# Kernel tuning notes

Measured on AMD Instinct MI355X. Metric: run time of the kernel, lower is better.

## Reference

```python
import jax, jax.numpy as jnp
import numpy as np

# ---- fixed architecture constants (from init_kwargs) ----
N_WALL, N_ROOF, N_WINDOW = 4, 1, 2
N_RC = N_WALL + N_ROOF
HID = 32
ENC_LEN = 48
DT = 900.0
R_OPAQUE, C_OPAQUE = 10.0, 1.0e5
R_TRANS = 2.0
DIRECT_COEF, ABS_WALL_COEF, ABS_ROOF_COEF = 0.5, 0.5, 0.5
C_ZONE = 1.0e5
B, T = 2048, 1440


def setup_inputs() -> dict:
    key = jax.random.key(0)
    k0, k1, k2 = jax.random.split(key, 3)
    input_X = jax.random.normal(k0, (B, T, 7), dtype=jnp.float32)
    # EnvelopeRC deterministic inits
    rc_R_inv = jnp.concatenate([
        1.0 / (10.0 + 1.0 * jnp.arange(N_WALL, dtype=jnp.float32)),
        1.0 / (20.0 + 2.0 * jnp.arange(N_ROOF, dtype=jnp.float32))])
    rc_C_inv = jnp.concatenate([
        1.0 / (80.0 + 10.0 * jnp.arange(N_WALL, dtype=jnp.float32)),
        1.0 / (60.0 + 10.0 * jnp.arange(N_ROOF, dtype=jnp.float32))])
    window_R_inv = 1.0 / (1.0 + 0.1 * jnp.arange(N_WINDOW, dtype=jnp.float32))
    # Internal MLP: xavier_uniform with gain 0.1, zero bias
    lim1 = 0.1 * np.sqrt(6.0 / (2 + HID))
    int_W1 = jax.random.uniform(k1, (HID, 2), jnp.float32, -lim1, lim1)
    int_b1 = jnp.zeros((HID,), jnp.float32)
    lim2 = 0.1 * np.sqrt(6.0 / (HID + 1))
    int_W2 = jax.random.uniform(k2, (1, HID), jnp.float32, -lim2, lim2)
    int_b2 = jnp.zeros((1,), jnp.float32)
    return {
        'input_X': input_X,
        'rc_R_inv': rc_R_inv, 'rc_C_inv': rc_C_inv, 'window_R_inv': window_R_inv,
        'hvac_gain': jnp.float32(0.1),
        'int_W1': int_W1, 'int_b1': int_b1, 'int_W2': int_W2, 'int_b2': int_b2,
        'int_gain': jnp.float32(0.1),
        'direct_gain': jnp.float32(0.1), 'abs_wall': jnp.float32(0.1), 'abs_roof': jnp.float32(0.1),
        'zone_C_inv': jnp.float32(1.0 / 10000.0),
    }


def _forward(input_X, rc_R_inv, rc_C_inv, window_R_inv, hvac_gain,
             int_W1, int_b1, int_W2, int_b2, int_gain,
             direct_gain, abs_wall, abs_roof, zone_C_inv):
    sp = jax.nn.softplus
    Bn, Tn = input_X.shape[0], input_X.shape[1]
    tz_gt  = input_X[:, :, 0]   # [B,T]
    t_amb  = input_X[:, :, 1]
    sol    = input_X[:, :, 2]
    int_x  = input_X[:, :, 3:6]
    hvac_x = input_X[:, :, 6]

    # Internal MLP (state-free -> vectorized over time)
    h1  = jax.nn.relu(jnp.einsum('bti,hi->bth', int_x[:, :, :2], int_W1) + int_b1)
    sch = jax.nn.sigmoid(jnp.einsum('bth,oh->bto', h1, int_W2) + int_b2)[:, :, 0] + int_x[:, :, 2]
    q_int  = sp(int_gain) * 0.1 * sch          # [B,T]
    q_hvac = sp(hvac_gain) * 0.1 * hvac_x      # [B,T]

    # Bounded RC parameters
    r_inv   = sp(rc_R_inv) * (1.0 / R_OPAQUE)  # [n_rc]
    c_inv   = sp(rc_C_inv) * (1.0 / C_OPAQUE)  # [n_rc]
    win_rsum = jnp.sum(sp(window_R_inv)) * (1.0 / R_TRANS)
    abs_rc  = jnp.where(jnp.arange(N_RC) < N_WALL,
                        sp(abs_wall) * ABS_WALL_COEF,
                        sp(abs_roof) * ABS_ROOF_COEF)   # [n_rc]
    q_dir   = sp(direct_gain) * DIRECT_COEF * sol       # [B,T]
    cz_inv  = sp(zone_C_inv) * (1.0 / C_ZONE)

    # Initial state: Tmid_i = 0.7*Tzone0 + 0.3*Tamb0
    Tz0   = tz_gt[:, 0]                                      # [B]
    Tmid0 = jnp.broadcast_to((0.7 * Tz0 + 0.3 * t_amb[:, 0])[:, None], (Bn, N_RC))

    # Teacher forcing during encoder window: carry GT zone temp while t+1 < enc_len
    tz_gt_next = jnp.concatenate([tz_gt[:, 1:], tz_gt[:, -1:]], axis=1)  # [B,T]
    use_gt = (jnp.arange(Tn) + 1) < ENC_LEN                              # [T]

    xs = (t_amb.T, sol.T, q_dir.T, q_int.T, q_hvac.T, tz_gt_next.T, use_gt)

    def step(carry, x):
        Tz, Tmid = carry                      # [B], [B,n_rc]
        ta, so, qd, qi, qh, gt_next, ug = x
        q_in  = (ta[:, None] - Tmid) * r_inv
        q_out = (Tmid - Tz[:, None]) * r_inv
        dTmid = (q_in - q_out + so[:, None] * abs_rc) * c_inv
        q_env = jnp.sum(q_out, axis=1) + (ta - Tz) * win_rsum
        dTz   = (q_env + qi + qh + qd) * cz_inv
        Tz_new   = Tz + dTz * DT
        Tmid_new = Tmid + dTmid * DT
        Tz_carry = jnp.where(ug, gt_next, Tz_new)
        return (Tz_carry, Tmid_new), Tz_new

    _, tz_seq = jax.lax.scan(step, (Tz0, Tmid0), xs)   # [T,B]
    return jnp.transpose(tz_seq)[:, :, None]           # [B,T,1]


def reference(input_X, rc_R_inv, rc_C_inv, window_R_inv, hvac_gain,
              int_W1, int_b1, int_W2, int_b2, int_gain,
              direct_gain, abs_wall, abs_roof, zone_C_inv):
    return _forward(input_X, rc_R_inv, rc_C_inv, window_R_inv, hvac_gain,
                    int_W1, int_b1, int_W2, int_b2, int_gain,
                    direct_gain, abs_wall, abs_roof, zone_C_inv)
```

## Files before the change

### kernel.cpp

```cpp
#include <hip/hip_runtime.h>
#include <math.h>

#define BATCH 2048
#define TLEN  1440
#define NC    30
#define CL    48

#define PACK_OFF 0
#define E_OFF    (BATCH*TLEN*4)
#define XC_OFF   (E_OFF + NC*6*BATCH)
#define A48_OFF  (XC_OFF + BATCH*NC*6)
#define VCOL_OFF (A48_OFF + 64)
#define PRM_OFF  (VCOL_OFF + 320)
#define WS_FLOATS (PRM_OFF + 32)

__device__ __forceinline__ float sp_precise(float x) { return log1pf(expf(x)); }

__global__ void k0_params(const float* __restrict__ rcR, const float* __restrict__ rcC,
                          const float* __restrict__ winR, const float* __restrict__ hvg,
                          const float* __restrict__ ing, const float* __restrict__ dg,
                          const float* __restrict__ aw, const float* __restrict__ ar,
                          const float* __restrict__ zc, float* __restrict__ ws) {
  __shared__ float A0s[36], Ma[36], Mb[36], M16[36], vbuf[2][8];
  int ln = threadIdx.x;
  float r[5], cc[5];
  #pragma unroll
  for (int j = 0; j < 5; ++j) { r[j] = sp_precise(rcR[j]) * 0.1f; cc[j] = sp_precise(rcC[j]) * 1e-5f; }
  float w    = (sp_precise(winR[0]) + sp_precise(winR[1])) * 0.5f;
  float cz   = sp_precise(zc[0]) * 1e-5f;
  float aW   = sp_precise(aw[0]) * 0.5f, aR = sp_precise(ar[0]) * 0.5f;
  float dtcz = 900.f * cz;
  if (ln == 0) {
    float* prm = ws + PRM_OFF;
    float rsum = 0.f;
    for (int j = 0; j < 5; ++j) {
      float P = 900.f * r[j] * cc[j];
      prm[j]      = P;
      prm[5 + j]  = 1.f - 2.f * P;
      prm[10 + j] = 900.f * cc[j] * ((j < 4) ? aW : aR);
      prm[15 + j] = dtcz * r[j];
      rsum += r[j];
    }
    prm[20] = 1.f - dtcz * (w + rsum);
    prm[21] = dtcz * w;
    prm[22] = dtcz;
    prm[23] = sp_precise(ing[0]) * 0.1f;
    prm[24] = sp_precise(hvg[0]) * 0.1f;
    prm[25] = sp_precise(dg[0])  * 0.5f;
    for (int i = 0; i < 36; ++i) A0s[i] = 0.f;
    A0s[0] = prm[20];
    for (int j = 0; j < 5; ++j) {
      A0s[0 * 6 + 1 + j]       = dtcz * r[j];
      A0s[(1 + j) * 6 + 0]     = prm[j];
      A0s[(1 + j) * 6 + 1 + j] = prm[5 + j];
    }
  }
  __syncthreads();
  int i6 = ln / 6, j6 = ln % 6;
  bool act = ln < 36;
#define MM(DST, L, R) { if (act) { float s = 0.f; \
  for (int m = 0; m < 6; ++m) s = fmaf((L)[i6 * 6 + m], (R)[m * 6 + j6], s); \
  (DST)[ln] = s; } __syncthreads(); }
  MM(Mb, A0s, A0s);
  MM(Ma, Mb, Mb);
  MM(Mb, Ma, Ma);
  MM(Ma, Mb, Mb);
  if (act) M16[ln] = Ma[ln];
  __syncthreads();
  MM(Mb, Ma, Ma);
  MM(Ma, Mb, M16);
  if (act) ws[A48_OFF + ln] = Ma[ln];
  if (ln < 6) vbuf[0][ln] = A0s[ln];
  __syncthreads();
  int cur = 0;
  for (int k = 0; k < CL; ++k) {
    if (ln < 6) {
      ws[VCOL_OFF + ln * CL + k] = vbuf[cur][ln];
      float s = 0.f;
      for (int m = 0; m < 6; ++m) s = fmaf(vbuf[cur][m], A0s[m * 6 + ln], s);
      vbuf[1 - cur][ln] = s;
    }
    __syncthreads();
    cur ^= 1;
  }
}

__global__ __launch_bounds__(256) void k1_pack(const float* __restrict__ X,
    const float* __restrict__ W1, const float* __restrict__ B1,
    const float* __restrict__ W2, const float* __restrict__ B2,
    float* __restrict__ ws) {
  int tid = blockIdx.x * 256 + threadIdx.x;
  const float* prm = ws + PRM_OFF;
  float dtczw = prm[21], dtcz = prm[22], cInt = prm[23], cHv = prm[24], cDir = prm[25];
  const float* x = X + (size_t)tid * 7;
  float ta = x[1], so = x[2], x3 = x[3], x4 = x[4], x5 = x[5], hv = x[6];
  float acc = B2[0];
  #pragma unroll
  for (int h = 0; h < 32; ++h) {
    float z = fmaf(W1[2 * h], x3, fmaf(W1[2 * h + 1], x4, B1[h]));
    acc = fmaf(W2[h], fmaxf(z, 0.f), acc);
  }
  float sch = __frcp_rn(1.f + __expf(-acc)) + x5;
  float q = fmaf(cInt, sch, fmaf(cHv, hv, cDir * so));
  float u = fmaf(dtczw, ta, dtcz * q);
  int b = tid / TLEN;
  int t = tid - b * TLEN;
  float gt = (t < 47) ? x[7] : 0.f;
  ((float4*)(ws + PACK_OFF))[tid] = make_float4(ta, so, u, gt);
}

__global__ __launch_bounds__(256) void k2a_scan(const float* __restrict__ X,
                                                float* __restrict__ out,
                                                float* __restrict__ ws) {
  int tid = blockIdx.x * 256 + threadIdx.x;
  int c = tid >> 11;
  int b = tid & (BATCH - 1);
  const float* prm = ws + PRM_OFF;
  float P0 = prm[0], P1 = prm[1], P2 = prm[2], P3 = prm[3], P4 = prm[4];
  float M0 = prm[5], M1 = prm[6], M2 = prm[7], M3 = prm[8], M4 = prm[9];
  float Q0 = prm[10], Q1 = prm[11], Q2 = prm[12], Q3 = prm[13], Q4 = prm[14];
  float K0 = prm[15], K1 = prm[16], K2 = prm[17], K3 = prm[18], K4 = prm[19];
  float AZ = prm[20];
  float Tz, T0, T1, T2, T3, T4;
  bool isc0 = (c == 0);
  if (isc0) {
    float tz0 = X[(size_t)b * (TLEN * 7)];
    float ta0 = X[(size_t)b * (TLEN * 7) + 1];
    Tz = tz0;
    float tm = fmaf(0.7f, tz0, 0.3f * ta0);
    T0 = T1 = T2 = T3 = T4 = tm;
  } else {
    Tz = 0.f; T0 = T1 = T2 = T3 = T4 = 0.f;
  }
  const float4* pk = ((const float4*)(ws + PACK_OFF)) + (size_t)b * TLEN + c * CL;
  float* op = out + (size_t)b * TLEN + c * CL;
  float ob0 = 0.f, ob1 = 0.f, ob2 = 0.f, ob3 = 0.f;
  #pragma unroll 4
  for (int k = 0; k < CL; ++k) {
    float4 f = pk[k];
    float d = fmaf(K0, T0, f.z);
    d = fmaf(K1, T1, d); d = fmaf(K2, T2, d); d = fmaf(K3, T3, d); d = fmaf(K4, T4, d);
    float tzn = fmaf(AZ, Tz, d);
    T0 = fmaf(M0, T0, fmaf(P0, Tz, fmaf(P0, f.x, Q0 * f.y)));
    T1 = fmaf(M1, T1, fmaf(P1, Tz, fmaf(P1, f.x, Q1 * f.y)));
    T2 = fmaf(M2, T2, fmaf(P2, Tz, fmaf(P2, f.x, Q2 * f.y)));
    T3 = fmaf(M3, T3, fmaf(P3, Tz, fmaf(P3, f.x, Q3 * f.y)));
    T4 = fmaf(M4, T4, fmaf(P4, Tz, fmaf(P4, f.x, Q4 * f.y)));
    int ph = k & 3;
    if (ph == 0) ob0 = tzn;
    else if (ph == 1) ob1 = tzn;
    else if (ph == 2) ob2 = tzn;
    else {
      ob3 = tzn;
      ((float4*)op)[k >> 2] = make_float4(ob0, ob1, ob2, ob3);
    }
    Tz = (isc0 && k < 47) ? f.w : tzn;
  }
  float* e = ws + E_OFF + (size_t)c * 6 * BATCH + b;
  e[0] = Tz;
  e[BATCH] = T0; e[2 * BATCH] = T1; e[3 * BATCH] = T2; e[4 * BATCH] = T3; e[5 * BATCH] = T4;
}

__global__ __launch_bounds__(256) void k2b_combine(float* __restrict__ ws) {
  int b = blockIdx.x * 256 + threadIdx.x;
  __shared__ float A48s[36];
  if (threadIdx.x < 36) A48s[threadIdx.x] = ws[A48_OFF + threadIdx.x];
  __syncthreads();
  const float* e = ws + E_OFF;
  float Xs[6];
  #pragma unroll
  for (int j = 0; j < 6; ++j) Xs[j] = e[j * BATCH + b];
  float* xc = ws + XC_OFF + (size_t)b * NC * 6;
  for (int c = 1; c < NC; ++c) {
    #pragma unroll
    for (int j = 0; j < 6; ++j) xc[c * 6 + j] = Xs[j];
    if (c < NC - 1) {
      float Y[6];
      #pragma unroll
      for (int i = 0; i < 6; ++i) {
        float s = e[((size_t)c * 6 + i) * BATCH + b];
        #pragma unroll
        for (int m = 0; m < 6; ++m) s = fmaf(A48s[i * 6 + m], Xs[m], s);
        Y[i] = s;
      }
      #pragma unroll
      for (int j = 0; j < 6; ++j) Xs[j] = Y[j];
    }
  }
}

__global__ __launch_bounds__(256) void k2c_correct(float* __restrict__ out,
                                                   const float* __restrict__ ws) {
  __shared__ float V[6 * CL];
  for (int i = threadIdx.x; i < 6 * CL; i += 256) V[i] = ws[VCOL_OFF + i];
  __syncthreads();
  int tid = blockIdx.x * 256 + threadIdx.x;
  int b = tid / (TLEN - CL);
  int tt = tid - b * (TLEN - CL);
  int t = tt + CL;
  int c = t / CL;
  int kk = t - c * CL;
  const float* xc = ws + XC_OFF + ((size_t)b * NC + c) * 6;
  float s = out[(size_t)b * TLEN + t];
  #pragma unroll
  for (int j = 0; j < 6; ++j) s = fmaf(V[j * CL + kk], xc[j], s);
  out[(size_t)b * TLEN + t] = s;
}

__global__ void k_fallback(const float* __restrict__ X,
    const float* __restrict__ rcR, const float* __restrict__ rcC,
    const float* __restrict__ winR, const float* __restrict__ hvg,
    const float* __restrict__ W1, const float* __restrict__ B1,
    const float* __restrict__ W2, const float* __restrict__ B2,
    const float* __restrict__ ing, const float* __restrict__ dg,
    const float* __restrict__ aw, const float* __restrict__ ar,
    const float* __restrict__ zc, float* __restrict__ out) {
  int b = blockIdx.x * 64 + threadIdx.x;
  if (b >= BATCH) return;
  float r[5], cc[5], P[5], M[5], Q[5], K[5];
  float rsum = 0.f;
  for (int j = 0; j < 5; ++j) { r[j] = sp_precise(rcR[j]) * 0.1f; cc[j] = sp_precise(rcC[j]) * 1e-5f; rsum += r[j]; }
  float w = (sp_precise(winR[0]) + sp_precise(winR[1])) * 0.5f;
  float cz = sp_precise(zc[0]) * 1e-5f;
  float aW = sp_precise(aw[0]) * 0.5f, aR = sp_precise(ar[0]) * 0.5f;
  float dtcz = 900.f * cz;
  for (int j = 0; j < 5; ++j) {
    P[j] = 900.f * r[j] * cc[j]; M[j] = 1.f - 2.f * P[j];
    Q[j] = 900.f * cc[j] * ((j < 4) ? aW : aR); K[j] = dtcz * r[j];
  }
  float AZ = 1.f - dtcz * (w + rsum), dtczw = dtcz * w;
  float cInt = sp_precise(ing[0]) * 0.1f, cHv = sp_precise(hvg[0]) * 0.1f, cDir = sp_precise(dg[0]) * 0.5f;
  const float* xb = X + (size_t)b * (TLEN * 7);
  float Tz = xb[0];
  float tm = fmaf(0.7f, xb[0], 0.3f * xb[1]);
  float Tm[5] = {tm, tm, tm, tm, tm};
  for (int t = 0; t < TLEN; ++t) {
    const float* x = xb + t * 7;
    float ta = x[1], so = x[2], x3 = x[3], x4 = x[4], x5 = x[5], hv = x[6];
    float acc = B2[0];
    #pragma unroll
    for (int h = 0; h < 32; ++h) {
      float z = fmaf(W1[2 * h], x3, fmaf(W1[2 * h + 1], x4, B1[h]));
      acc = fmaf(W2[h], fmaxf(z, 0.f), acc);
    }
    float sch = __frcp_rn(1.f + __expf(-acc)) + x5;
    float q = fmaf(cInt, sch, fmaf(cHv, hv, cDir * so));
    float u = fmaf(dtczw, ta, dtcz * q);
    float d = u;
    #pragma unroll
    for (int j = 0; j < 5; ++j) d = fmaf(K[j], Tm[j], d);
    float tzn = fmaf(AZ, Tz, d);
    #pragma unroll
    for (int j = 0; j < 5; ++j)
      Tm[j] = fmaf(M[j], Tm[j], fmaf(P[j], Tz, fmaf(P[j], ta, Q[j] * so)));
    out[(size_t)b * TLEN + t] = tzn;
    Tz = (t < 47) ? x[7] : tzn;
  }
}

extern "C" void kernel_launch(void* const* d_in, const int* in_sizes, int n_in,
                              void* d_out, int out_size, void* d_ws, size_t ws_size,
                              hipStream_t stream) {
  const float* X    = (const float*)d_in[0];
  const float* rcR  = (const float*)d_in[1];
  const float* rcC  = (const float*)d_in[2];
  const float* winR = (const float*)d_in[3];
  const float* hvg  = (const float*)d_in[4];
  const float* W1   = (const float*)d_in[5];
  const float* B1   = (const float*)d_in[6];
  const float* W2   = (const float*)d_in[7];
  const float* B2   = (const float*)d_in[8];
  const float* ing  = (const float*)d_in[9];
  const float* dg   = (const float*)d_in[10];
  const float* aw   = (const float*)d_in[11];
  const float* ar   = (const float*)d_in[12];
  const float* zc   = (const float*)d_in[13];
  float* out = (float*)d_out;
  float* ws  = (float*)d_ws;

  if (ws_size >= (size_t)WS_FLOATS * sizeof(float)) {
    k0_params<<<1, 64, 0, stream>>>(rcR, rcC, winR, hvg, ing, dg, aw, ar, zc, ws);
    k1_pack<<<(BATCH * TLEN) / 256, 256, 0, stream>>>(X, W1, B1, W2, B2, ws);
    k2a_scan<<<(BATCH * NC) / 256, 256, 0, stream>>>(X, out, ws);
    k2b_combine<<<BATCH / 256, 256, 0, stream>>>(ws);
    k2c_correct<<<(BATCH * (TLEN - CL)) / 256, 256, 0, stream>>>(out, ws);
  } else {
    k_fallback<<<BATCH / 64, 64, 0, stream>>>(X, rcR, rcC, winR, hvg, W1, B1, W2, B2,
                                              ing, dg, aw, ar, zc, out);
  }
}
```

Measured before the change: 209.5 us.

## Fuse MLP pack stage into chunked scan kernel, dropping packed intermediate buffer

The per-timestep MLP and input packing kernel is folded into the chunked scan kernel. The scan now reads the raw input directly and computes the drive term inline, with parameters rebuilt per thread from the raw weights. This removes a full write and read of a large float4 workspace buffer and one kernel launch. In exchange, the MLP work runs inside the low-parallelism scan kernel, and each thread now makes strided scalar loads of the input rows, which may expose latency.

Result: slower. 221.3 us (+5.6%).

```diff
diff --git a/kernel.cpp b/kernel.cpp
--- a/kernel.cpp
+++ b/kernel.cpp
@@ -6,8 +6,7 @@
 #define NC    30
 #define CL    48
 
-#define PACK_OFF 0
-#define E_OFF    (BATCH*TLEN*4)
+#define E_OFF    0
 #define XC_OFF   (E_OFF + NC*6*BATCH)
 #define A48_OFF  (XC_OFF + BATCH*NC*6)
 #define VCOL_OFF (A48_OFF + 64)
@@ -15,6 +14,43 @@
 #define WS_FLOATS (PRM_OFF + 32)
 
 __device__ __forceinline__ float sp_precise(float x) { return log1pf(expf(x)); }
+
+struct Prm {
+  float P[5], M[5], Q[5], K[5];
+  float AZ, dtczw, dtcz, cInt, cHv, cDir;
+};
+__device__ __forceinline__ Prm make_prm(const float* rcR, const float* rcC,
+                                        const float* winR, const float* hvg,
+                                        const float* ing, const float* dg,
+                                        const float* aw, const float* ar,
+                                        const float* zc) {
+  Prm p;
+  float r[5], cc[5], rsum = 0.f;
+  #pragma unroll
+  for (int j = 0; j < 5; ++j) {
+    r[j] = sp_precise(rcR[j]) * 0.1f;
+    cc[j] = sp_precise(rcC[j]) * 1e-5f;
+    rsum += r[j];
+  }
+  float w  = (sp_precise(winR[0]) + sp_precise(winR[1])) * 0.5f;
+  float cz = sp_precise(zc[0]) * 1e-5f;
+  float aW = sp_precise(aw[0]) * 0.5f, aR = sp_precise(ar[0]) * 0.5f;
+  float dtcz = 900.f * cz;
+  #pragma unroll
+  for (int j = 0; j < 5; ++j) {
+    p.P[j] = 900.f * r[j] * cc[j];
+    p.M[j] = 1.f - 2.f * p.P[j];
+    p.Q[j] = 900.f * cc[j] * ((j < 4) ? aW : aR);
+    p.K[j] = dtcz * r[j];
+  }
+  p.AZ = 1.f - dtcz * (w + rsum);
+  p.dtczw = dtcz * w;
+  p.dtcz = dtcz;
+  p.cInt = sp_precise(ing[0]) * 0.1f;
+  p.cHv  = sp_precise(hvg[0]) * 0.1f;
+  p.cDir = sp_precise(dg[0])  * 0.5f;
+  return p;
+}
 
 __global__ void k0_params(const float* __restrict__ rcR, const float* __restrict__ rcC,
                           const float* __restrict__ winR, const float* __restrict__ hvg,
@@ -23,36 +59,14 @@
                           const float* __restrict__ zc, float* __restrict__ ws) {
   __shared__ float A0s[36], Ma[36], Mb[36], M16[36], vbuf[2][8];
   int ln = threadIdx.x;
-  float r[5], cc[5];
-  #pragma unroll
-  for (int j = 0; j < 5; ++j) { r[j] = sp_precise(rcR[j]) * 0.1f; cc[j] = sp_precise(rcC[j]) * 1e-5f; }
-  float w    = (sp_precise(winR[0]) + sp_precise(winR[1])) * 0.5f;
-  float cz   = sp_precise(zc[0]) * 1e-5f;
-  float aW   = sp_precise(aw[0]) * 0.5f, aR = sp_precise(ar[0]) * 0.5f;
-  float dtcz = 900.f * cz;
   if (ln == 0) {
-    float* prm = ws + PRM_OFF;
-    float rsum = 0.f;
+    Prm p = make_prm(rcR, rcC, winR, hvg, ing, dg, aw, ar, zc);
+    for (int i = 0; i < 36; ++i) A0s[i] = 0.f;
+    A0s[0] = p.AZ;
     for (int j = 0; j < 5; ++j) {
-      float P = 900.f * r[j] * cc[j];
-      prm[j]      = P;
-      prm[5 + j]  = 1.f - 2.f * P;
-      prm[10 + j] = 900.f * cc[j] * ((j < 4) ? aW : aR);
-      prm[15 + j] = dtcz * r[j];
-      rsum += r[j];
-    }
-    prm[20] = 1.f - dtcz * (w + rsum);
-    prm[21] = dtcz * w;
-    prm[22] = dtcz;
-    prm[23] = sp_precise(ing[0]) * 0.1f;
-    prm[24] = sp_precise(hvg[0]) * 0.1f;
-    prm[25] = sp_precise(dg[0])  * 0.5f;
-    for (int i = 0; i < 36; ++i) A0s[i] = 0.f;
-    A0s[0] = prm[20];
-    for (int j = 0; j < 5; ++j) {
-      A0s[0 * 6 + 1 + j]       = dtcz * r[j];
-      A0s[(1 + j) * 6 + 0]     = prm[j];
-      A0s[(1 + j) * 6 + 1 + j] = prm[5 + j];
+      A0s[0 * 6 + 1 + j]       = p.K[j];
+      A0s[(1 + j) * 6 + 0]     = p.P[j];
+      A0s[(1 + j) * 6 + 1 + j] = p.M[j];
     }
   }
   __syncthreads();
@@ -85,80 +99,67 @@
   }
 }
 
-__global__ __launch_bounds__(256) void k1_pack(const float* __restrict__ X,
+__global__ __launch_bounds__(256) void kb_scan(const float* __restrict__ X,
+    const float* __restrict__ rcR, const float* __restrict__ rcC,
+    const float* __restrict__ winR, const float* __restrict__ hvg,
     const float* __restrict__ W1, const float* __restrict__ B1,
     const float* __restrict__ W2, const float* __restrict__ B2,
-    float* __restrict__ ws) {
-  int tid = blockIdx.x * 256 + threadIdx.x;
-  const float* prm = ws + PRM_OFF;
-  float dtczw = prm[21], dtcz = prm[22], cInt = prm[23], cHv = prm[24], cDir = prm[25];
-  const float* x = X + (size_t)tid * 7;
-  float ta = x[1], so = x[2], x3 = x[3], x4 = x[4], x5 = x[5], hv = x[6];
-  float acc = B2[0];
-  #pragma unroll
-  for (int h = 0; h < 32; ++h) {
-    float z = fmaf(W1[2 * h], x3, fmaf(W1[2 * h + 1], x4, B1[h]));
-    acc = fmaf(W2[h], fmaxf(z, 0.f), acc);
-  }
-  float sch = __frcp_rn(1.f + __expf(-acc)) + x5;
-  float q = fmaf(cInt, sch, fmaf(cHv, hv, cDir * so));
-  float u = fmaf(dtczw, ta, dtcz * q);
-  int b = tid / TLEN;
-  int t = tid - b * TLEN;
-  float gt = (t < 47) ? x[7] : 0.f;
-  ((float4*)(ws + PACK_OFF))[tid] = make_float4(ta, so, u, gt);
-}
-
-__global__ __launch_bounds__(256) void k2a_scan(const float* __restrict__ X,
-                                                float* __restrict__ out,
-                                                float* __restrict__ ws) {
+    const float* __restrict__ ing, const float* __restrict__ dg,
+    const float* __restrict__ aw, const float* __restrict__ ar,
+    const float* __restrict__ zc,
+    float* __restrict__ out, float* __restrict__ ws) {
   int tid = blockIdx.x * 256 + threadIdx.x;
   int c = tid >> 11;
   int b = tid & (BATCH - 1);
-  const float* prm = ws + PRM_OFF;
-  float P0 = prm[0], P1 = prm[1], P2 = prm[2], P3 = prm[3], P4 = prm[4];
-  float M0 = prm[5], M1 = prm[6], M2 = prm[7], M3 = prm[8], M4 = prm[9];
-  float Q0 = prm[10], Q1 = prm[11], Q2 = prm[12], Q3 = prm[13], Q4 = prm[14];
-  float K0 = prm[15], K1 = prm[16], K2 = prm[17], K3 = prm[18], K4 = prm[19];
-  float AZ = prm[20];
+  Prm p = make_prm(rcR, rcC, winR, hvg, ing, dg, aw, ar, zc);
+  float b2 = B2[0];
+
   float Tz, T0, T1, T2, T3, T4;
   bool isc0 = (c == 0);
+  const float* xb = X + ((size_t)b * TLEN + c * CL) * 7;
   if (isc0) {
-    float tz0 = X[(size_t)b * (TLEN * 7)];
-    float ta0 = X[(size_t)b * (TLEN * 7) + 1];
+    float tz0 = xb[0], ta0 = xb[1];
     Tz = tz0;
     float tm = fmaf(0.7f, tz0, 0.3f * ta0);
     T0 = T1 = T2 = T3 = T4 = tm;
   } else {
-    Tz = 0.f; T0 = T1 = T2 = T3 = T4 = 0.f;
-  }
-  const float4* pk = ((const float4*)(ws + PACK_OFF)) + (size_t)b * TLEN + c * CL;
+    Tz = T0 = T1 = T2 = T3 = T4 = 0.f;
+  }
   float* op = out + (size_t)b * TLEN + c * CL;
-  float ob0 = 0.f, ob1 = 0.f, ob2 = 0.f, ob3 = 0.f;
+  float ob0 = 0.f, ob1 = 0.f, ob2 = 0.f;
   #pragma unroll 4
   for (int k = 0; k < CL; ++k) {
-    float4 f = pk[k];
-    float d = fmaf(K0, T0, f.z);
-    d = fmaf(K1, T1, d); d = fmaf(K2, T2, d); d = fmaf(K3, T3, d); d = fmaf(K4, T4, d);
-    float tzn = fmaf(AZ, Tz, d);
-    T0 = fmaf(M0, T0, fmaf(P0, Tz, fmaf(P0, f.x, Q0 * f.y)));
-    T1 = fmaf(M1, T1, fmaf(P1, Tz, fmaf(P1, f.x, Q1 * f.y)));
-    T2 = fmaf(M2, T2, fmaf(P2, Tz, fmaf(P2, f.x, Q2 * f.y)));
-    T3 = fmaf(M3, T3, fmaf(P3, Tz, fmaf(P3, f.x, Q3 * f.y)));
-    T4 = fmaf(M4, T4, fmaf(P4, Tz, fmaf(P4, f.x, Q4 * f.y)));
+    const float* x = xb + k * 7;
+    float ta = x[1], so = x[2], x3 = x[3], x4 = x[4], x5 = x[5], hv = x[6];
+    float acc = b2;
+    #pragma unroll
+    for (int h = 0; h < 32; ++h) {
+      float z = fmaf(W1[2 * h], x3, fmaf(W1[2 * h + 1], x4, B1[h]));
+      acc = fmaf(W2[h], fmaxf(z, 0.f), acc);
+    }
+    float sch = __frcp_rn(1.f + __expf(-acc)) + x5;
+    float q = fmaf(p.cInt, sch, fmaf(p.cHv, hv, p.cDir * so));
+    float u = fmaf(p.dtczw, ta, p.dtcz * q);
+    float d = fmaf(p.K[0], T0, u);
+    d = fmaf(p.K[1], T1, d); d = fmaf(p.K[2], T2, d);
+    d = fmaf(p.K[3], T3, d); d = fmaf(p.K[4], T4, d);
+    float tzn = fmaf(p.AZ, Tz, d);
+    T0 = fmaf(p.M[0], T0, fmaf(p.P[0], Tz, fmaf(p.P[0], ta, p.Q[0] * so)));
+    T1 = fmaf(p.M[1], T1, fmaf(p.P[1], Tz, fmaf(p.P[1], ta, p.Q[1] * so)));
+    T2 = fmaf(p.M[2], T2, fmaf(p.P[2], Tz, fmaf(p.P[2], ta, p.Q[2] * so)));
+    T3 = fmaf(p.M[3], T3, fmaf(p.P[3], Tz, fmaf(p.P[3], ta, p.Q[3] * so)));
+    T4 = fmaf(p.M[4], T4, fmaf(p.P[4], Tz, fmaf(p.P[4], ta, p.Q[4] * so)));
     int ph = k & 3;
     if (ph == 0) ob0 = tzn;
     else if (ph == 1) ob1 = tzn;
     else if (ph == 2) ob2 = tzn;
-    else {
-      ob3 = tzn;
-      ((float4*)op)[k >> 2] = make_float4(ob0, ob1, ob2, ob3);
-    }
-    Tz = (isc0 && k < 47) ? f.w : tzn;
+    else ((float4*)op)[k >> 2] = make_float4(ob0, ob1, ob2, tzn);
+    Tz = (isc0 && k < 47) ? x[7] : tzn;
   }
   float* e = ws + E_OFF + (size_t)c * 6 * BATCH + b;
   e[0] = Tz;
-  e[BATCH] = T0; e[2 * BATCH] = T1; e[3 * BATCH] = T2; e[4 * BATCH] = T3; e[5 * BATCH] = T4;
+  e[BATCH] = T0; e[2 * BATCH] = T1; e[3 * BATCH] = T2;
+  e[4 * BATCH] = T3; e[5 * BATCH] = T4;
 }
 
 __global__ __launch_bounds__(256) void k2b_combine(float* __restrict__ ws) {
@@ -217,19 +218,7 @@
     const float* __restrict__ zc, float* __restrict__ out) {
   int b = blockIdx.x * 64 + threadIdx.x;
   if (b >= BATCH) return;
-  float r[5], cc[5], P[5], M[5], Q[5], K[5];
-  float rsum = 0.f;
-  for (int j = 0; j < 5; ++j) { r[j] = sp_precise(rcR[j]) * 0.1f; cc[j] = sp_precise(rcC[j]) * 1e-5f; rsum += r[j]; }
-  float w = (sp_precise(winR[0]) + sp_precise(winR[1])) * 0.5f;
-  float cz = sp_precise(zc[0]) * 1e-5f;
-  float aW = sp_precise(aw[0]) * 0.5f, aR = sp_precise(ar[0]) * 0.5f;
-  float dtcz = 900.f * cz;
-  for (int j = 0; j < 5; ++j) {
-    P[j] = 900.f * r[j] * cc[j]; M[j] = 1.f - 2.f * P[j];
-    Q[j] = 900.f * cc[j] * ((j < 4) ? aW : aR); K[j] = dtcz * r[j];
-  }
-  float AZ = 1.f - dtcz * (w + rsum), dtczw = dtcz * w;
-  float cInt = sp_precise(ing[0]) * 0.1f, cHv = sp_precise(hvg[0]) * 0.1f, cDir = sp_precise(dg[0]) * 0.5f;
+  Prm p = make_prm(rcR, rcC, winR, hvg, ing, dg, aw, ar, zc);
   const float* xb = X + (size_t)b * (TLEN * 7);
   float Tz = xb[0];
   float tm = fmaf(0.7f, xb[0], 0.3f * xb[1]);
@@ -244,15 +233,15 @@
       acc = fmaf(W2[h], fmaxf(z, 0.f), acc);
     }
     float sch = __frcp_rn(1.f + __expf(-acc)) + x5;
-    float q = fmaf(cInt, sch, fmaf(cHv, hv, cDir * so));
-    float u = fmaf(dtczw, ta, dtcz * q);
+    float q = fmaf(p.cInt, sch, fmaf(p.cHv, hv, p.cDir * so));
+    float u = fmaf(p.dtczw, ta, p.dtcz * q);
     float d = u;
     #pragma unroll
-    for (int j = 0; j < 5; ++j) d = fmaf(K[j], Tm[j], d);
-    float tzn = fmaf(AZ, Tz, d);
+    for (int j = 0; j < 5; ++j) d = fmaf(p.K[j], Tm[j], d);
+    float tzn = fmaf(p.AZ, Tz, d);
     #pragma unroll
     for (int j = 0; j < 5; ++j)
-      Tm[j] = fmaf(M[j], Tm[j], fmaf(P[j], Tz, fmaf(P[j], ta, Q[j] * so)));
+      Tm[j] = fmaf(p.M[j], Tm[j], fmaf(p.P[j], Tz, fmaf(p.P[j], ta, p.Q[j] * so)));
     out[(size_t)b * TLEN + t] = tzn;
     Tz = (t < 47) ? x[7] : tzn;
   }
@@ -280,8 +269,9 @@
 
   if (ws_size >= (size_t)WS_FLOATS * sizeof(float)) {
     k0_params<<<1, 64, 0, stream>>>(rcR, rcC, winR, hvg, ing, dg, aw, ar, zc, ws);
-    k1_pack<<<(BATCH * TLEN) / 256, 256, 0, stream>>>(X, W1, B1, W2, B2, ws);
-    k2a_scan<<<(BATCH * NC) / 256, 256, 0, stream>>>(X, out, ws);
+    kb_scan<<<(BATCH * NC) / 256, 256, 0, stream>>>(X, rcR, rcC, winR, hvg,
+                                                    W1, B1, W2, B2, ing, dg, aw, ar, zc,
+                                                    out, ws);
     k2b_combine<<<BATCH / 256, 256, 0, stream>>>(ws);
     k2c_correct<<<(BATCH * (TLEN - CL)) / 256, 256, 0, stream>>>(out, ws);
   } else {
```
